# Kernel optimization log

Hardware: AMD Instinct MI355X
Metric: run time of the kernel (lower is better)

## Reference

```python
import jax, jax.numpy as jnp
import numpy as np

B, S, HID, MEM, NW = 32, 256, 1024, 256, 1024
PLAST, IMP = 0.1, 1.0
W_SCALE = 0.02  # sane init for projection weights


def setup_inputs() -> dict:
    key = jax.random.key(0)
    ks = jax.random.split(key, 24)
    n = lambda k, sh, s=1.0: jax.random.normal(k, sh, dtype=jnp.float32) * s
    inp = {
        "q": n(ks[0], (B, S, HID)),
        "data": n(ks[1], (NW, HID)),
        "episodic_k": n(ks[2], (MEM, HID)),
        "episodic_v": n(ks[3], (MEM, HID)),
        "semantic_k": n(ks[4], (MEM, HID)),
        "semantic_v": n(ks[5], (MEM, HID)),
        "working_m": n(ks[6], (1, 10, HID)),
    }
    i = 7
    for name in ("atte", "atts", "attw"):
        inp[name + "_in_w"] = n(ks[i], (3 * HID, HID), W_SCALE); i += 1
        inp[name + "_in_b"] = jnp.zeros((3 * HID,), jnp.float32)
        inp[name + "_out_w"] = n(ks[i], (HID, HID), W_SCALE); i += 1
        inp[name + "_out_b"] = jnp.zeros((HID,), jnp.float32)
    inp["proj_w"] = n(ks[i], (HID, 3 * HID), W_SCALE)
    inp["proj_b"] = jnp.zeros((HID,), jnp.float32)
    return inp


def mha_shared_kv(q, k, v, in_w, in_b, out_w, out_b, n_heads):
    # q: [B,S,H]; k,v: [M,H] (memory bank shared across the batch)
    d = q.shape[-1] // n_heads
    wq, wk, wv = jnp.split(in_w, 3, axis=0)
    bq, bk, bv = jnp.split(in_b, 3)
    Bq, Sq, _ = q.shape
    M = k.shape[0]
    qh = (q @ wq.T + bq).reshape(Bq, Sq, n_heads, d)   # [B,S,h,d]
    kh = (k @ wk.T + bk).reshape(M, n_heads, d)        # [M,h,d]
    vh = (v @ wv.T + bv).reshape(M, n_heads, d)
    scale = 1.0 / jnp.sqrt(jnp.float32(d))
    att = jax.nn.softmax(jnp.einsum('bshd,mhd->bhsm', qh, kh) * scale, axis=-1)
    o = jnp.einsum('bhsm,mhd->bshd', att, vh).reshape(Bq, Sq, -1)
    return o @ out_w.T + out_b


def reference(q, data, episodic_k, episodic_v, semantic_k, semantic_v, working_m,
              atte_in_w, atte_in_b, atte_out_w, atte_out_b,
              atts_in_w, atts_in_b, atts_out_w, atts_out_b,
              attw_in_w, attw_in_b, attw_out_w, attw_out_b,
              proj_w, proj_b):
    # ---- write(data, 'episodic'): softmax-addressed fast-weight update ----
    probs = jax.nn.softmax(data @ episodic_k.T, axis=-1)          # [N,M]
    w = probs * (PLAST * IMP)                                     # [N,M]
    u = w.mean(axis=0)[:, None]                                   # [M,1] mean update strength per slot
    writes = jnp.einsum('nm,nh->mh', w, data) / NW                # mean_n data[n]*w[n,m]
    ek = jax.lax.stop_gradient(episodic_k * (1.0 - u) + writes)   # .data assignment -> no grad
    ev = jax.lax.stop_gradient(episodic_v * (1.0 - u) + writes)
    # ---- read(q): 3 small attentions over memory banks, concat, project ----
    e_r = mha_shared_kv(q, ek, ev, atte_in_w, atte_in_b, atte_out_w, atte_out_b, 16)
    s_r = mha_shared_kv(q, semantic_k, semantic_v, atts_in_w, atts_in_b, atts_out_w, atts_out_b, 16)
    w_r = mha_shared_kv(q, working_m[0], working_m[0], attw_in_w, attw_in_b, attw_out_w, attw_out_b, 8)
    cat = jnp.concatenate((e_r, s_r, w_r), axis=-1)               # [B,S,3H]
    return cat @ proj_w.T + proj_b                                # [B,S,H]
```

## Files before the change

kernel.cpp:

```cpp
#include <hip/hip_runtime.h>
#include <hip/hip_bf16.h>


using bf = __hip_bfloat16;
using short8v = __attribute__((ext_vector_type(8))) short;
using f32x4  = __attribute__((ext_vector_type(4))) float;

#define GLOAD_LDS16(g, l) __builtin_amdgcn_global_load_lds( \
    (const __attribute__((address_space(1))) void*)(g), \
    (__attribute__((address_space(3))) void*)(l), 16, 0, 0)

__device__ inline float bf2f(unsigned short s) {
    union { unsigned u; float f; } c; c.u = ((unsigned)s) << 16; return c.f;
}
__device__ inline unsigned short f2bu(float x) {
    union { float f; unsigned u; } c; c.f = x;
    unsigned r = c.u + 0x7FFF + ((c.u >> 16) & 1);
    return (unsigned short)(r >> 16);
}
__device__ inline void storeC(float* p, float v) { *p = v; }
__device__ inline void storeC(bf* p, float v) { *p = __float2bfloat16(v); }

__global__ __launch_bounds__(256) void gemm_bt(
    const bf* __restrict__ A, int lda,
    const bf* __restrict__ B, int ldb,
    float* __restrict__ part, int M, int N, int K)
{
    __shared__ short As[128 * 64];
    __shared__ short Bs[128 * 64];
    const int nbn = N >> 7;
    const int bm = blockIdx.x / nbn, bn = blockIdx.x % nbn;
    const int t = threadIdx.x;
    const int w = t >> 6, lane = t & 63;
    const int wr = w >> 1, wc = w & 1;
    const int l16 = lane & 15, lhi = lane >> 4;
    const int kc = K / gridDim.y;
    const int kbeg = blockIdx.y * kc, kend = kbeg + kc;

    f32x4 acc[4][4];
    #pragma unroll
    for (int i = 0; i < 4; ++i)
        #pragma unroll
        for (int j = 0; j < 4; ++j) { f32x4 z = {0.f, 0.f, 0.f, 0.f}; acc[i][j] = z; }

    const bf* Arow = A + (size_t)bm * 128 * lda;
    const bf* Brow = B + (size_t)bn * 128 * ldb;

    for (int k0 = kbeg; k0 < kend; k0 += 64) {
        #pragma unroll
        for (int j = 0; j < 4; ++j) {
            int u = (w * 4 + j) * 64 + lane;
            int row = u >> 3, c8 = u & 7;
            int slot = c8 ^ (row & 7);
            GLOAD_LDS16(Brow + (size_t)row * ldb + k0 + slot * 8, &Bs[(w * 4 + j) * 512]);
            GLOAD_LDS16(Arow + (size_t)row * lda + k0 + slot * 8, &As[(w * 4 + j) * 512]);
        }
        __syncthreads();
        #pragma unroll
        for (int kk = 0; kk < 2; ++kk) {
            short8v af[4], bfr[4];
            #pragma unroll
            for (int mt = 0; mt < 4; ++mt) {
                int row = wr * 64 + mt * 16 + l16;
                int slot = (kk * 4 + lhi) ^ (row & 7);
                af[mt] = *(const short8v*)&As[row * 64 + slot * 8];
            }
            #pragma unroll
            for (int nt = 0; nt < 4; ++nt) {
                int row = wc * 64 + nt * 16 + l16;
                int slot = (kk * 4 + lhi) ^ (row & 7);
                bfr[nt] = *(const short8v*)&Bs[row * 64 + slot * 8];
            }
            #pragma unroll
            for (int mt = 0; mt < 4; ++mt)
                #pragma unroll
                for (int nt = 0; nt < 4; ++nt)
                    acc[mt][nt] = __builtin_amdgcn_mfma_f32_16x16x32_bf16(
                        af[mt], bfr[nt], acc[mt][nt], 0, 0, 0);
        }
        __syncthreads();
    }
    #pragma unroll
    for (int mt = 0; mt < 4; ++mt)
        #pragma unroll
        for (int nt = 0; nt < 4; ++nt) {
            int col = bn * 128 + wc * 64 + nt * 16 + l16;
            #pragma unroll
            for (int j = 0; j < 4; ++j) {
                int rowg = bm * 128 + wr * 64 + mt * 16 + lhi * 4 + j;
                part[(size_t)blockIdx.y * M * N + (size_t)rowg * N + col] = acc[mt][nt][j];
            }
        }
}

template <typename CT>
__global__ __launch_bounds__(512) void gemm256(
    const bf* __restrict__ A, int lda,
    const bf* __restrict__ B, int ldb,
    const float* __restrict__ bias,
    CT* __restrict__ C, int ldc,
    int M, int N, int K)
{
    __shared__ short As[256 * 64];
    __shared__ short Bs[128 * 64];
    const int nbn = N >> 7;
    int bid = blockIdx.x;
    bid = (bid & 7) * (gridDim.x >> 3) + (bid >> 3);
    const int bm = bid / nbn, bn = bid % nbn;
    const int t = threadIdx.x;
    const int w = t >> 6, lane = t & 63;
    const int wr = w >> 1, wc = w & 1;
    const int l16 = lane & 15, lhi = lane >> 4;

    f32x4 acc[4][4];
    #pragma unroll
    for (int i = 0; i < 4; ++i)
        #pragma unroll
        for (int j = 0; j < 4; ++j) { f32x4 z = {0.f, 0.f, 0.f, 0.f}; acc[i][j] = z; }

    const bf* Arow = A + (size_t)bm * 256 * lda;
    const bf* Brow = B + (size_t)bn * 128 * ldb;

    for (int k0 = 0; k0 < K; k0 += 64) {
        #pragma unroll
        for (int j = 0; j < 2; ++j) {
            int u = t + (j << 9);
            int row = u >> 3, c8 = u & 7;
            int slot = c8 ^ (row & 7);
            GLOAD_LDS16(Brow + (size_t)row * ldb + k0 + slot * 8, &Bs[(j * 8 + w) * 512]);
        }
        #pragma unroll
        for (int j = 0; j < 4; ++j) {
            int u = t + (j << 9);
            int row = u >> 3, c8 = u & 7;
            int slot = c8 ^ (row & 7);
            GLOAD_LDS16(Arow + (size_t)row * lda + k0 + slot * 8, &As[(j * 8 + w) * 512]);
        }
        __syncthreads();
        #pragma unroll
        for (int kk = 0; kk < 2; ++kk) {
            short8v af[4], bfr[4];
            #pragma unroll
            for (int mt = 0; mt < 4; ++mt) {
                int row = wr * 64 + mt * 16 + l16;
                int slot = (kk * 4 + lhi) ^ (row & 7);
                af[mt] = *(const short8v*)&As[row * 64 + slot * 8];
            }
            #pragma unroll
            for (int nt = 0; nt < 4; ++nt) {
                int row = wc * 64 + nt * 16 + l16;
                int slot = (kk * 4 + lhi) ^ (row & 7);
                bfr[nt] = *(const short8v*)&Bs[row * 64 + slot * 8];
            }
            #pragma unroll
            for (int mt = 0; mt < 4; ++mt)
                #pragma unroll
                for (int nt = 0; nt < 4; ++nt)
                    acc[mt][nt] = __builtin_amdgcn_mfma_f32_16x16x32_bf16(
                        af[mt], bfr[nt], acc[mt][nt], 0, 0, 0);
        }
        __syncthreads();
    }
    #pragma unroll
    for (int mt = 0; mt < 4; ++mt)
        #pragma unroll
        for (int nt = 0; nt < 4; ++nt) {
            int col = bn * 128 + wc * 64 + nt * 16 + l16;
            float bv = bias ? bias[col] : 0.0f;
            #pragma unroll
            for (int j = 0; j < 4; ++j) {
                int rowg = bm * 256 + wr * 64 + mt * 16 + lhi * 4 + j;
                storeC(&C[(size_t)rowg * ldc + col], acc[mt][nt][j] + bv);
            }
        }
}

__global__ __launch_bounds__(512) void gemm256db(
    const bf* __restrict__ A, int lda,
    const bf* __restrict__ B, int ldb,
    const float* __restrict__ bias,
    float* __restrict__ C, int ldc,
    int M, int N, int K)
{
    __shared__ short As0[256 * 64];
    __shared__ short Bs0[128 * 64];
    __shared__ short As1[256 * 64];
    __shared__ short Bs1[128 * 64];
    const int nbn = N >> 7;
    int bid = blockIdx.x;
    bid = (bid & 7) * (gridDim.x >> 3) + (bid >> 3);
    const int bm = bid / nbn, bn = bid % nbn;
    const int t = threadIdx.x;
    const int w = t >> 6, lane = t & 63;
    const int wr = w >> 1, wc = w & 1;
    const int l16 = lane & 15, lhi = lane >> 4;

    f32x4 acc[4][4];
    #pragma unroll
    for (int i = 0; i < 4; ++i)
        #pragma unroll
        for (int j = 0; j < 4; ++j) { f32x4 z = {0.f, 0.f, 0.f, 0.f}; acc[i][j] = z; }

    const bf* Arow = A + (size_t)bm * 256 * lda;
    const bf* Brow = B + (size_t)bn * 128 * ldb;

    auto stage = [&](short* Asd, short* Bsd, int k0) {
        #pragma unroll
        for (int j = 0; j < 2; ++j) {
            int u = t + (j << 9);
            int row = u >> 3, c8 = u & 7;
            int slot = c8 ^ (row & 7);
            GLOAD_LDS16(Brow + (size_t)row * ldb + k0 + slot * 8, &Bsd[(j * 8 + w) * 512]);
        }
        #pragma unroll
        for (int j = 0; j < 4; ++j) {
            int u = t + (j << 9);
            int row = u >> 3, c8 = u & 7;
            int slot = c8 ^ (row & 7);
            GLOAD_LDS16(Arow + (size_t)row * lda + k0 + slot * 8, &Asd[(j * 8 + w) * 512]);
        }
    };
    auto compute = [&](const short* Ass, const short* Bss) {
        #pragma unroll
        for (int kk = 0; kk < 2; ++kk) {
            short8v af[4], bfr[4];
            #pragma unroll
            for (int mt = 0; mt < 4; ++mt) {
                int row = wr * 64 + mt * 16 + l16;
                int slot = (kk * 4 + lhi) ^ (row & 7);
                af[mt] = *(const short8v*)&Ass[row * 64 + slot * 8];
            }
            #pragma unroll
            for (int nt = 0; nt < 4; ++nt) {
                int row = wc * 64 + nt * 16 + l16;
                int slot = (kk * 4 + lhi) ^ (row & 7);
                bfr[nt] = *(const short8v*)&Bss[row * 64 + slot * 8];
            }
            #pragma unroll
            for (int mt = 0; mt < 4; ++mt)
                #pragma unroll
                for (int nt = 0; nt < 4; ++nt)
                    acc[mt][nt] = __builtin_amdgcn_mfma_f32_16x16x32_bf16(
                        af[mt], bfr[nt], acc[mt][nt], 0, 0, 0);
        }
    };

    const int nt_ = K >> 6;
    stage(As0, Bs0, 0);
    stage(As1, Bs1, 64);
    asm volatile("s_waitcnt vmcnt(6)" ::: "memory");
    __builtin_amdgcn_sched_barrier(0);
    __builtin_amdgcn_s_barrier();

    for (int ti = 0; ti < nt_ - 2; ti += 2) {
        compute(As0, Bs0);
        __builtin_amdgcn_s_barrier();
        stage(As0, Bs0, (ti + 2) << 6);
        asm volatile("s_waitcnt vmcnt(6)" ::: "memory");
        __builtin_amdgcn_sched_barrier(0);
        __builtin_amdgcn_s_barrier();
        compute(As1, Bs1);
        __builtin_amdgcn_s_barrier();
        stage(As1, Bs1, (ti + 3) << 6);
        asm volatile("s_waitcnt vmcnt(6)" ::: "memory");
        __builtin_amdgcn_sched_barrier(0);
        __builtin_amdgcn_s_barrier();
    }
    compute(As0, Bs0);
    __builtin_amdgcn_s_barrier();
    asm volatile("s_waitcnt vmcnt(0)" ::: "memory");
    __builtin_amdgcn_sched_barrier(0);
    __builtin_amdgcn_s_barrier();
    compute(As1, Bs1);

    #pragma unroll
    for (int mt = 0; mt < 4; ++mt)
        #pragma unroll
        for (int nt = 0; nt < 4; ++nt) {
            int col = bn * 128 + wc * 64 + nt * 16 + l16;
            float bv = bias ? bias[col] : 0.0f;
            #pragma unroll
            for (int j = 0; j < 4; ++j) {
                int rowg = bm * 256 + wr * 64 + mt * 16 + lhi * 4 + j;
                C[(size_t)rowg * ldc + col] = acc[mt][nt][j] + bv;
            }
        }
}

struct GG { const bf* A; const bf* B; const float* bias; bf* out;
            int lda, ldb, M, N, ldo, xoff; };
struct GG7 { GG g[7]; };

__global__ __launch_bounds__(256) void ggemm(GG7 P)
{
    __shared__ short As[128 * 64];
    __shared__ short Bs[128 * 64];
    const int bid = blockIdx.x;
    int gidx = 0;
    #pragma unroll
    for (int i = 1; i < 7; ++i) if (bid >= P.g[i].xoff) gidx = i;
    const GG d = P.g[gidx];
    const int lb = bid - d.xoff;
    const int nbn = d.N >> 7;
    const int bm = lb / nbn, bn = lb % nbn;
    const int t = threadIdx.x;
    const int w = t >> 6, lane = t & 63;
    const int wr = w >> 1, wc = w & 1;
    const int l16 = lane & 15, lhi = lane >> 4;

    f32x4 acc[4][4];
    #pragma unroll
    for (int i = 0; i < 4; ++i)
        #pragma unroll
        for (int j = 0; j < 4; ++j) { f32x4 z = {0.f, 0.f, 0.f, 0.f}; acc[i][j] = z; }

    const bf* Afrow = d.A + (size_t)bm * 128 * d.lda;
    const bf* Brow  = d.B + (size_t)bn * 128 * d.ldb;

    for (int k0 = 0; k0 < 1024; k0 += 64) {
        #pragma unroll
        for (int j = 0; j < 4; ++j) {
            int u = (w * 4 + j) * 64 + lane;
            int row = u >> 3, c8 = u & 7;
            int slot = c8 ^ (row & 7);
            GLOAD_LDS16(Brow + (size_t)row * d.ldb + k0 + slot * 8, &Bs[(w * 4 + j) * 512]);
            GLOAD_LDS16(Afrow + (size_t)row * d.lda + k0 + slot * 8, &As[(w * 4 + j) * 512]);
        }
        __syncthreads();
        #pragma unroll
        for (int kk = 0; kk < 2; ++kk) {
            short8v af[4], bfr[4];
            #pragma unroll
            for (int mt = 0; mt < 4; ++mt) {
                int row = wr * 64 + mt * 16 + l16;
                int slot = (kk * 4 + lhi) ^ (row & 7);
                af[mt] = *(const short8v*)&As[row * 64 + slot * 8];
            }
            #pragma unroll
            for (int nt = 0; nt < 4; ++nt) {
                int row = wc * 64 + nt * 16 + l16;
                int slot = (kk * 4 + lhi) ^ (row & 7);
                bfr[nt] = *(const short8v*)&Bs[row * 64 + slot * 8];
            }
            #pragma unroll
            for (int mt = 0; mt < 4; ++mt)
                #pragma unroll
                for (int nt = 0; nt < 4; ++nt)
                    acc[mt][nt] = __builtin_amdgcn_mfma_f32_16x16x32_bf16(
                        af[mt], bfr[nt], acc[mt][nt], 0, 0, 0);
        }
        __syncthreads();
    }
    #pragma unroll
    for (int mt = 0; mt < 4; ++mt)
        #pragma unroll
        for (int nt = 0; nt < 4; ++nt) {
            int col = bn * 128 + wc * 64 + nt * 16 + l16;
            float bv = d.bias ? d.bias[col] : 0.0f;
            #pragma unroll
            for (int j = 0; j < 4; ++j) {
                int rowg = bm * 128 + wr * 64 + mt * 16 + lhi * 4 + j;
                d.out[(size_t)rowg * d.ldo + col]
                    = __float2bfloat16(acc[mt][nt][j] + bv);
            }
        }
}

__global__ __launch_bounds__(512) void attn_es(
    bf* Ocat, const bf* __restrict__ khE, const bf* __restrict__ khS,
    const bf* __restrict__ vTE, const bf* __restrict__ vTS)
{
    __shared__ short Ks[256 * 64];
    __shared__ short Vs[64 * 256];
    const int bank = blockIdx.x >> 10;
    const int lbid = blockIdx.x & 1023;
    const bf* kh  = bank ? khS : khE;
    const bf* vhT = bank ? vTS : vTE;
    bf* QO = Ocat + bank * 1024;
    const int qt = lbid >> 4, head = lbid & 15;
    const int t = threadIdx.x, w = t >> 6, lane = t & 63;
    const int l16 = lane & 15, lhi = lane >> 4;
    const float scale = 0.125f;

    #pragma unroll
    for (int j = 0; j < 4; ++j) {
        int ublk = w * 4 + j;
        int u = ublk * 64 + lane;
        { int row = u >> 3, c8 = u & 7;
          int slot = c8 ^ (row & 7);
          GLOAD_LDS16(kh + (size_t)row * 1024 + head * 64 + slot * 8, &Ks[ublk * 512]); }
        { int row = u >> 5, c16 = u & 31;
          int slot = c16 ^ (row & 7);
          GLOAD_LDS16(vhT + (size_t)(head * 64 + row) * 256 + slot * 8, &Vs[ublk * 512]); }
    }
    const int qr = qt * 128 + w * 16 + l16;
    short8v aq0 = *(const short8v*)(QO + (size_t)qr * 3072 + head * 64 + lhi * 8);
    short8v aq1 = *(const short8v*)(QO + (size_t)qr * 3072 + head * 64 + 32 + lhi * 8);
    __syncthreads();

    f32x4 sc[16];
    #pragma unroll
    for (int nt = 0; nt < 16; ++nt) { f32x4 z = {0.f, 0.f, 0.f, 0.f}; sc[nt] = z; }
    #pragma unroll
    for (int nt = 0; nt < 16; ++nt) {
        int row = nt * 16 + l16;
        #pragma unroll
        for (int kk = 0; kk < 2; ++kk) {
            int slot = (kk * 4 + lhi) ^ (row & 7);
            short8v b = *(const short8v*)&Ks[row * 64 + slot * 8];
            sc[nt] = __builtin_amdgcn_mfma_f32_16x16x32_bf16(kk ? aq1 : aq0, b, sc[nt], 0, 0, 0);
        }
    }
    float inv[4];
    #pragma unroll
    for (int j = 0; j < 4; ++j) {
        float m_ = -1e30f;
        #pragma unroll
        for (int nt = 0; nt < 16; ++nt) m_ = fmaxf(m_, sc[nt][j]);
        #pragma unroll
        for (int off = 8; off; off >>= 1) m_ = fmaxf(m_, __shfl_xor(m_, off));
        float s_ = 0.f;
        #pragma unroll
        for (int nt = 0; nt < 16; ++nt) {
            float e = __expf((sc[nt][j] - m_) * scale);
            sc[nt][j] = e; s_ += e;
        }
        #pragma unroll
        for (int off = 8; off; off >>= 1) s_ += __shfl_xor(s_, off);
        inv[j] = 1.0f / s_;
    }
    __syncthreads();

    char* Pw = (char*)Ks + w * 4096;
    f32x4 oa[4];
    #pragma unroll
    for (int nt = 0; nt < 4; ++nt) { f32x4 z = {0.f, 0.f, 0.f, 0.f}; oa[nt] = z; }
    #pragma unroll
    for (int h = 0; h < 2; ++h) {
        #pragma unroll
        for (int nt = 0; nt < 8; ++nt) {
            int colL = nt * 16 + l16;
            #pragma unroll
            for (int j = 0; j < 4; ++j) {
                int row = lhi * 4 + j;
                *(short*)(Pw + row * 256 + ((colL * 2) ^ ((row & 7) << 4)))
                    = (short)f2bu(sc[h * 8 + nt][j] * inv[j]);
            }
        }
        #pragma unroll
        for (int kk = 0; kk < 4; ++kk) {
            short8v a = *(const short8v*)(Pw + l16 * 256 + (((kk * 32 + lhi * 8) * 2) ^ ((l16 & 7) << 4)));
            #pragma unroll
            for (int nt = 0; nt < 4; ++nt) {
                int row = nt * 16 + l16;
                int m = h * 128 + kk * 32 + lhi * 8;
                short8v b = *(const short8v*)((const char*)Vs + row * 512 + ((m * 2) ^ ((row & 7) << 4)));
                oa[nt] = __builtin_amdgcn_mfma_f32_16x16x32_bf16(a, b, oa[nt], 0, 0, 0);
            }
        }
    }
    #pragma unroll
    for (int nt = 0; nt < 4; ++nt)
        #pragma unroll
        for (int j = 0; j < 4; ++j)
            QO[(size_t)(qt * 128 + w * 16 + lhi * 4 + j) * 3072 + head * 64 + nt * 16 + l16]
                = __float2bfloat16(oa[nt][j]);
}

__global__ __launch_bounds__(256) void attn_w(
    bf* QOp, const bf* __restrict__ khw, const bf* __restrict__ vhw)
{
    const int bs = blockIdx.x;
    const int t = threadIdx.x;
    const int head = t >> 5;
    const int dg = head * 128 + (t & 31) * 4;

    ushort4 qv = *(const ushort4*)(QOp + (size_t)bs * 3072 + dg);
    float q0 = bf2f(qv.x), q1 = bf2f(qv.y), q2 = bf2f(qv.z), q3 = bf2f(qv.w);
    float s[10];
    #pragma unroll
    for (int m = 0; m < 10; ++m) {
        ushort4 kv = *(const ushort4*)(khw + (size_t)m * 1024 + dg);
        float pr = q0 * bf2f(kv.x) + q1 * bf2f(kv.y) + q2 * bf2f(kv.z) + q3 * bf2f(kv.w);
        #pragma unroll
        for (int off = 16; off; off >>= 1) pr += __shfl_xor(pr, off);
        s[m] = pr * 0.08838834764831845f;
    }
    float mx = s[0];
    #pragma unroll
    for (int m = 1; m < 10; ++m) mx = fmaxf(mx, s[m]);
    float pp[10], sum = 0.f;
    #pragma unroll
    for (int m = 0; m < 10; ++m) { pp[m] = __expf(s[m] - mx); sum += pp[m]; }
    float inv = 1.0f / sum;
    float o0 = 0, o1 = 0, o2 = 0, o3 = 0;
    #pragma unroll
    for (int m = 0; m < 10; ++m) {
        ushort4 vv = *(const ushort4*)(vhw + (size_t)m * 1024 + dg);
        o0 += pp[m] * bf2f(vv.x); o1 += pp[m] * bf2f(vv.y);
        o2 += pp[m] * bf2f(vv.z); o3 += pp[m] * bf2f(vv.w);
    }
    bf* op = QOp + (size_t)bs * 3072 + dg;
    op[0] = __float2bfloat16(o0 * inv); op[1] = __float2bfloat16(o1 * inv);
    op[2] = __float2bfloat16(o2 * inv); op[3] = __float2bfloat16(o3 * inv);
}

struct CS { const float* src; bf* dst; int voff; };
struct MP {
    CS cs[13];
    const float* tsrc[4]; bf* tdst[4];
    const float* ow[3]; const float* ob[3]; const float* ib[3];
    float* bp;
    const float* inb_e; const float* inb_s; float* bqcat3;
    const float* wm; const float* inw_w; const float* inb_w;
    bf* khw; bf* vhw;
};

__global__ __launch_bounds__(256) void megaprep(MP P)
{
    __shared__ unsigned short tile[64][65];
    const int bid = blockIdx.x;
    const int t = threadIdx.x;
    if (bid < 20224) {
        int gi = bid * 256 + t;
        int gidx = 0;
        #pragma unroll
        for (int i = 1; i < 13; ++i) if (gi >= P.cs[i].voff) gidx = i;
        int i = (gi - P.cs[gidx].voff) * 4;
        float4 v = *(const float4*)(P.cs[gidx].src + i);
        ushort4 o;
        o.x = f2bu(v.x); o.y = f2bu(v.y); o.z = f2bu(v.z); o.w = f2bu(v.w);
        *(ushort4*)((unsigned short*)P.cs[gidx].dst + i) = o;
    } else if (bid < 21248) {
        int lb = bid - 20224;
        int sel = lb >> 8, bb = lb & 255;
        const float* in = P.tsrc[sel];
        bf* outT = P.tdst[sel];
        int bx = bb & 15, by = bb >> 4;
        int r0 = by * 64, c0 = bx * 64;
        int tr = t >> 4, tc4 = (t & 15) * 4;
        #pragma unroll
        for (int i = 0; i < 4; ++i) {
            int r = tr + i * 16;
            float4 v = *(const float4*)(in + (size_t)(r0 + r) * 1024 + c0 + tc4);
            tile[r][tc4 + 0] = f2bu(v.x); tile[r][tc4 + 1] = f2bu(v.y);
            tile[r][tc4 + 2] = f2bu(v.z); tile[r][tc4 + 3] = f2bu(v.w);
        }
        __syncthreads();
        #pragma unroll
        for (int i = 0; i < 4; ++i) {
            int r = tr + i * 16;
            ushort4 v;
            v.x = tile[tc4 + 0][r]; v.y = tile[tc4 + 1][r];
            v.z = tile[tc4 + 2][r]; v.w = tile[tc4 + 3][r];
            *(ushort4*)((unsigned short*)outT + (size_t)(c0 + r) * 1024 + r0 + tc4) = v;
        }
    } else if (bid < 22016) {
        int g = (bid - 21248) * 4 + (t >> 6);
        int lane = t & 63;
        int bank = g >> 10, j = g & 1023;
        const float* ow = P.ow[bank];
        const float* xx = P.ib[bank] + 2048;
        const float* wrow = ow + (size_t)j * 1024;
        float acc = 0.f;
        #pragma unroll
        for (int cc = 0; cc < 4; ++cc) {
            float4 a = *(const float4*)(wrow + lane * 16 + cc * 4);
            float4 x = *(const float4*)(xx + lane * 16 + cc * 4);
            acc += a.x * x.x + a.y * x.y + a.z * x.z + a.w * x.w;
        }
        #pragma unroll
        for (int off = 32; off; off >>= 1) acc += __shfl_xor(acc, off);
        if (lane == 0) P.bp[g] = acc + P.ob[bank][j];
    } else if (bid < 22028) {
        int i = (bid - 22016) * 256 + t;
        if (i < 1024) P.bqcat3[i] = P.inb_e[i];
        else if (i < 2048) P.bqcat3[i] = P.inb_s[i - 1024];
        else P.bqcat3[i] = P.inb_w[i - 2048];
    } else {
        int o = (bid - 22028) * 4 + (t >> 6);
        int lane = t & 63;
        int sel = o >= 10240;
        int o2 = o - sel * 10240;
        int m = o2 >> 10, c = o2 & 1023;
        const float* wrow = P.inw_w + (size_t)(1024 + sel * 1024 + c) * 1024;
        const float* xrow = P.wm + (size_t)m * 1024;
        float acc = 0.f;
        #pragma unroll
        for (int cc = 0; cc < 4; ++cc) {
            float4 a = *(const float4*)(wrow + lane * 16 + cc * 4);
            float4 x = *(const float4*)(xrow + lane * 16 + cc * 4);
            acc += a.x * x.x + a.y * x.y + a.z * x.z + a.w * x.w;
        }
        #pragma unroll
        for (int off = 32; off; off >>= 1) acc += __shfl_xor(acc, off);
        if (lane == 0) {
            float v = acc + (sel ? 0.f : P.inb_w[1024 + c]);
            (sel ? P.vhw : P.khw)[(size_t)m * 1024 + c] = __float2bfloat16(v);
        }
    }
}


__global__ __launch_bounds__(256) void btot_kern(
    const float* __restrict__ bp, const float* __restrict__ pw,
    const float* __restrict__ pb, float* __restrict__ btot)
{
    int j = blockIdx.x * 4 + (threadIdx.x >> 6);
    int lane = threadIdx.x & 63;
    const float* row = pw + (size_t)j * 3072;
    float acc = 0.f;
    #pragma unroll
    for (int it = 0; it < 12; ++it) {
        int c = lane * 4 + it * 256;
        float4 a = *(const float4*)(row + c);
        float4 x = *(const float4*)(bp + c);
        acc += a.x * x.x + a.y * x.y + a.z * x.z + a.w * x.w;
    }
    #pragma unroll
    for (int off = 32; off; off >>= 1) acc += __shfl_xor(acc, off);
    if (lane == 0) btot[j] = acc + pb[j];
}

__global__ __launch_bounds__(256) void write_softmax_p(const float* __restrict__ part,
                                                       bf* __restrict__ wT)
{
    const int n = blockIdx.x, m = threadIdx.x;
    float s = 0.f;
    #pragma unroll
    for (int k = 0; k < 8; ++k) s += part[(size_t)k * 262144 + n * 256 + m];
    float mx = s;
    #pragma unroll
    for (int off = 32; off; off >>= 1) mx = fmaxf(mx, __shfl_xor(mx, off));
    __shared__ float red[4], red2[4];
    int w = threadIdx.x >> 6;
    if ((threadIdx.x & 63) == 0) red[w] = mx;
    __syncthreads();
    mx = fmaxf(fmaxf(red[0], red[1]), fmaxf(red[2], red[3]));
    float e = __expf(s - mx);
    float sm = e;
    #pragma unroll
    for (int off = 32; off; off >>= 1) sm += __shfl_xor(sm, off);
    if ((threadIdx.x & 63) == 0) red2[w] = sm;
    __syncthreads();
    sm = red2[0] + red2[1] + red2[2] + red2[3];
    wT[(size_t)m * 1024 + n] = __float2bfloat16(0.1f * e / sm);
}

__global__ __launch_bounds__(256) void usum_kern(const bf* __restrict__ wT, float* __restrict__ u)
{
    int w = threadIdx.x >> 6, lane = threadIdx.x & 63;
    int m = blockIdx.x * 4 + w;
    const bf* row = wT + (size_t)m * 1024;
    float s = 0.f;
    for (int i = lane; i < 1024; i += 64) s += __bfloat162float(row[i]);
    #pragma unroll
    for (int off = 32; off; off >>= 1) s += __shfl_xor(s, off);
    if (lane == 0) u[m] = s * (1.0f / 1024.0f);
}

__global__ __launch_bounds__(256) void update_fused(
    const float* __restrict__ epk, const float* __restrict__ epv,
    const float* __restrict__ u, const float* __restrict__ part,
    bf* __restrict__ ekb, bf* __restrict__ evb)
{
    int i = blockIdx.x * 256 + threadIdx.x;
    int m = i >> 10;
    float wr = 0.f;
    #pragma unroll
    for (int k = 0; k < 8; ++k) wr += part[(size_t)k * 262144 + i];
    wr *= (1.0f / 1024.0f);
    float f = 1.0f - u[m];
    ekb[i] = __float2bfloat16(epk[i] * f + wr);
    evb[i] = __float2bfloat16(epv[i] * f + wr);
}

extern "C" void kernel_launch(void* const* d_in, const int* in_sizes, int n_in,
                              void* d_out, int out_size, void* d_ws, size_t ws_size,
                              hipStream_t stream)
{
    const float* q     = (const float*)d_in[0];
    const float* data  = (const float*)d_in[1];
    const float* epk   = (const float*)d_in[2];
    const float* epv   = (const float*)d_in[3];
    const float* smk   = (const float*)d_in[4];
    const float* smv   = (const float*)d_in[5];
    const float* wm    = (const float*)d_in[6];
    const float* inw_e = (const float*)d_in[7];  const float* inb_e = (const float*)d_in[8];
    const float* ow_e  = (const float*)d_in[9];  const float* ob_e  = (const float*)d_in[10];
    const float* inw_s = (const float*)d_in[11]; const float* inb_s = (const float*)d_in[12];
    const float* ow_s  = (const float*)d_in[13]; const float* ob_s  = (const float*)d_in[14];
    const float* inw_w = (const float*)d_in[15]; const float* inb_w = (const float*)d_in[16];
    const float* ow_w  = (const float*)d_in[17]; const float* ob_w  = (const float*)d_in[18];
    const float* pw    = (const float*)d_in[19]; const float* pb    = (const float*)d_in[20];
    float* out  = (float*)d_out;
    float* part = (float*)d_out;
    bf* qb  = (bf*)((char*)d_out + 8388608);
    bf* pwb = (bf*)((char*)d_out + 25165824);

    char* p = (char*)d_ws;
    auto alloc = [&](size_t bytes) -> char* {
        char* r = p; p += (bytes + 255) & ~(size_t)255; return r;
    };
    float* u      = (float*)alloc(256 * 4);
    float* bp     = (float*)alloc(3072 * 4);
    float* btot   = (float*)alloc(1024 * 4);
    float* bqcat3 = (float*)alloc(3072 * 4);
    bf* wT     = (bf*)alloc(256 * 1024 * 2);
    bf* dT     = (bf*)alloc((size_t)1024 * 1024 * 2);
    bf* datab  = (bf*)alloc((size_t)1024 * 1024 * 2);
    bf* epkb   = (bf*)alloc(256 * 1024 * 2);
    bf* smkb   = (bf*)alloc(256 * 1024 * 2);
    bf* smvb   = (bf*)alloc(256 * 1024 * 2);
    bf* ekb    = (bf*)alloc(256 * 1024 * 2);
    bf* evb    = (bf*)alloc(256 * 1024 * 2);
    bf* khE    = (bf*)alloc(256 * 1024 * 2);
    bf* khS    = (bf*)alloc(256 * 1024 * 2);
    bf* vTE    = (bf*)alloc((size_t)1024 * 256 * 2);
    bf* vTS    = (bf*)alloc((size_t)1024 * 256 * 2);
    bf* khw    = (bf*)alloc(10 * 1024 * 2);
    bf* vhw    = (bf*)alloc(10 * 1024 * 2);
    bf* Wall   = (bf*)alloc((size_t)3072 * 1024 * 2);
    bf* WkE    = (bf*)alloc((size_t)1024 * 1024 * 2);
    bf* WkS    = (bf*)alloc((size_t)1024 * 1024 * 2);
    bf* WvE    = (bf*)alloc((size_t)1024 * 1024 * 2);
    bf* WvS    = (bf*)alloc((size_t)1024 * 1024 * 2);
    bf* owT0   = (bf*)alloc((size_t)1024 * 1024 * 2);
    bf* owT1   = (bf*)alloc((size_t)1024 * 1024 * 2);
    bf* owT2   = (bf*)alloc((size_t)1024 * 1024 * 2);
    bf* Gcat   = (bf*)alloc((size_t)1024 * 3072 * 2);
    bf* Ocat   = (bf*)alloc((size_t)8192 * 3072 * 2);
    if ((size_t)(p - (char*)d_ws) > ws_size) return;

    {
        MP P;
        CS cs[13] = { {q, qb, 0},
                      {epk,  epkb, 2097152}, {smv, smvb, 2162688},
                      {inw_e, Wall, 2228224},
                      {inw_s, Wall + (size_t)1024 * 1024, 2490368},
                      {inw_w, Wall + (size_t)2048 * 1024, 2752512},
                      {inw_e + (size_t)1024 * 1024, WkE, 3014656},
                      {inw_s + (size_t)1024 * 1024, WkS, 3276800},
                      {data, datab, 3538944},
                      {pw, pwb, 3801088},
                      {smk, smkb, 4587520},
                      {inw_e + (size_t)2048 * 1024, WvE, 4653056},
                      {inw_s + (size_t)2048 * 1024, WvS, 4915200} };
        for (int i = 0; i < 13; ++i) P.cs[i] = cs[i];
        P.tsrc[0] = data; P.tdst[0] = dT;
        P.tsrc[1] = ow_e; P.tdst[1] = owT0;
        P.tsrc[2] = ow_s; P.tdst[2] = owT1;
        P.tsrc[3] = ow_w; P.tdst[3] = owT2;
        P.ow[0] = ow_e; P.ow[1] = ow_s; P.ow[2] = ow_w;
        P.ob[0] = ob_e; P.ob[1] = ob_s; P.ob[2] = ob_w;
        P.ib[0] = inb_e; P.ib[1] = inb_s; P.ib[2] = inb_w;
        P.bp = bp;
        P.inb_e = inb_e; P.inb_s = inb_s; P.bqcat3 = bqcat3;
        P.wm = wm; P.inw_w = inw_w; P.inb_w = inb_w;
        P.khw = khw; P.vhw = vhw;
        megaprep<<<27148, 256, 0, stream>>>(P);
    }
    btot_kern<<<256, 256, 0, stream>>>(bp, pw, pb, btot);

    gemm_bt<<<dim3(16, 8), 256, 0, stream>>>(datab, 1024, epkb, 1024, part, 1024, 256, 1024);
    write_softmax_p<<<1024, 256, 0, stream>>>(part, wT);
    usum_kern<<<64, 256, 0, stream>>>(wT, u);
    gemm_bt<<<dim3(16, 8), 256, 0, stream>>>(wT, 1024, dT, 1024, part, 256, 1024, 1024);
    update_fused<<<1024, 256, 0, stream>>>(epk, epv, u, part, ekb, evb);

    gemm256<bf><<<768, 512, 0, stream>>>(
        qb, 1024, Wall, 1024, bqcat3, Ocat, 3072, 8192, 3072, 1024);

    {
        GG7 G = {{
            { ekb,        WkE,  inb_e + 1024, khE,         1024, 1024,  256, 1024, 1024, 0   },
            { smkb,       WkS,  inb_s + 1024, khS,         1024, 1024,  256, 1024, 1024, 16  },
            { WvE,        evb,  nullptr,      vTE,         1024, 1024, 1024,  256,  256, 32  },
            { WvS,        smvb, nullptr,      vTS,         1024, 1024, 1024,  256,  256, 48  },
            { pwb + 0,    owT0, nullptr,      Gcat + 0,    3072, 1024, 1024, 1024, 3072, 64  },
            { pwb + 1024, owT1, nullptr,      Gcat + 1024, 3072, 1024, 1024, 1024, 3072, 128 },
            { pwb + 2048, owT2, nullptr,      Gcat + 2048, 3072, 1024, 1024, 1024, 3072, 192 },
        }};
        ggemm<<<256, 256, 0, stream>>>(G);
    }

    attn_es<<<2048, 512, 0, stream>>>(Ocat, khE, khS, vTE, vTS);
    attn_w<<<8192, 256, 0, stream>>>(Ocat + 2048, khw, vhw);

    gemm256db<<<256, 512, 0, stream>>>(
        Ocat, 3072, Gcat, 3072, btot, out, 1024, 8192, 1024, 3072);
}
```

Measured before the change: 277.4 us.

## Use double-buffered GEMM for QKV, fuse usum into update, batch attn_w rows

Templates the double-buffered gemm256db kernel on its output type and uses it in place of the single-buffered gemm256 for the large Q projection GEMM, so global loads overlap MFMA work. The separate usum kernel is removed: update_fused now computes each slot's mean weight with a block reduction and applies the update with vectorised loads and stores, one block per memory slot. attn_w processes four rows per block and keeps the key and value registers loaded across them, cutting redundant loads and launching a quarter as many blocks. The cost is higher LDS use in the QKV GEMM, which may lower occupancy.

```diff
diff --git a/kernel.cpp b/kernel.cpp
--- a/kernel.cpp
+++ b/kernel.cpp
@@ -94,92 +94,11 @@
 }
 
 template <typename CT>
-__global__ __launch_bounds__(512) void gemm256(
+__global__ __launch_bounds__(512) void gemm256db(
     const bf* __restrict__ A, int lda,
     const bf* __restrict__ B, int ldb,
     const float* __restrict__ bias,
     CT* __restrict__ C, int ldc,
-    int M, int N, int K)
-{
-    __shared__ short As[256 * 64];
-    __shared__ short Bs[128 * 64];
-    const int nbn = N >> 7;
-    int bid = blockIdx.x;
-    bid = (bid & 7) * (gridDim.x >> 3) + (bid >> 3);
-    const int bm = bid / nbn, bn = bid % nbn;
-    const int t = threadIdx.x;
-    const int w = t >> 6, lane = t & 63;
-    const int wr = w >> 1, wc = w & 1;
-    const int l16 = lane & 15, lhi = lane >> 4;
-
-    f32x4 acc[4][4];
-    #pragma unroll
-    for (int i = 0; i < 4; ++i)
-        #pragma unroll
-        for (int j = 0; j < 4; ++j) { f32x4 z = {0.f, 0.f, 0.f, 0.f}; acc[i][j] = z; }
-
-    const bf* Arow = A + (size_t)bm * 256 * lda;
-    const bf* Brow = B + (size_t)bn * 128 * ldb;
-
-    for (int k0 = 0; k0 < K; k0 += 64) {
-        #pragma unroll
-        for (int j = 0; j < 2; ++j) {
-            int u = t + (j << 9);
-            int row = u >> 3, c8 = u & 7;
-            int slot = c8 ^ (row & 7);
-            GLOAD_LDS16(Brow + (size_t)row * ldb + k0 + slot * 8, &Bs[(j * 8 + w) * 512]);
-        }
-        #pragma unroll
-        for (int j = 0; j < 4; ++j) {
-            int u = t + (j << 9);
-            int row = u >> 3, c8 = u & 7;
-            int slot = c8 ^ (row & 7);
-            GLOAD_LDS16(Arow + (size_t)row * lda + k0 + slot * 8, &As[(j * 8 + w) * 512]);
-        }
-        __syncthreads();
-        #pragma unroll
-        for (int kk = 0; kk < 2; ++kk) {
-            short8v af[4], bfr[4];
-            #pragma unroll
-            for (int mt = 0; mt < 4; ++mt) {
-                int row = wr * 64 + mt * 16 + l16;
-                int slot = (kk * 4 + lhi) ^ (row & 7);
-                af[mt] = *(const short8v*)&As[row * 64 + slot * 8];
-            }
-            #pragma unroll
-            for (int nt = 0; nt < 4; ++nt) {
-                int row = wc * 64 + nt * 16 + l16;
-                int slot = (kk * 4 + lhi) ^ (row & 7);
-                bfr[nt] = *(const short8v*)&Bs[row * 64 + slot * 8];
-            }
-            #pragma unroll
-            for (int mt = 0; mt < 4; ++mt)
-                #pragma unroll
-                for (int nt = 0; nt < 4; ++nt)
-                    acc[mt][nt] = __builtin_amdgcn_mfma_f32_16x16x32_bf16(
-                        af[mt], bfr[nt], acc[mt][nt], 0, 0, 0);
-        }
-        __syncthreads();
-    }
-    #pragma unroll
-    for (int mt = 0; mt < 4; ++mt)
-        #pragma unroll
-        for (int nt = 0; nt < 4; ++nt) {
-            int col = bn * 128 + wc * 64 + nt * 16 + l16;
-            float bv = bias ? bias[col] : 0.0f;
-            #pragma unroll
-            for (int j = 0; j < 4; ++j) {
-                int rowg = bm * 256 + wr * 64 + mt * 16 + lhi * 4 + j;
-                storeC(&C[(size_t)rowg * ldc + col], acc[mt][nt][j] + bv);
-            }
-        }
-}
-
-__global__ __launch_bounds__(512) void gemm256db(
-    const bf* __restrict__ A, int lda,
-    const bf* __restrict__ B, int ldb,
-    const float* __restrict__ bias,
-    float* __restrict__ C, int ldc,
     int M, int N, int K)
 {
     __shared__ short As0[256 * 64];
@@ -282,7 +201,7 @@
             #pragma unroll
             for (int j = 0; j < 4; ++j) {
                 int rowg = bm * 256 + wr * 64 + mt * 16 + lhi * 4 + j;
-                C[(size_t)rowg * ldc + col] = acc[mt][nt][j] + bv;
+                storeC(&C[(size_t)rowg * ldc + col], acc[mt][nt][j] + bv);
             }
         }
 }
@@ -470,39 +389,47 @@
 __global__ __launch_bounds__(256) void attn_w(
     bf* QOp, const bf* __restrict__ khw, const bf* __restrict__ vhw)
 {
-    const int bs = blockIdx.x;
     const int t = threadIdx.x;
     const int head = t >> 5;
     const int dg = head * 128 + (t & 31) * 4;
 
-    ushort4 qv = *(const ushort4*)(QOp + (size_t)bs * 3072 + dg);
-    float q0 = bf2f(qv.x), q1 = bf2f(qv.y), q2 = bf2f(qv.z), q3 = bf2f(qv.w);
-    float s[10];
+    ushort4 kv[10], vv[10];
     #pragma unroll
     for (int m = 0; m < 10; ++m) {
-        ushort4 kv = *(const ushort4*)(khw + (size_t)m * 1024 + dg);
-        float pr = q0 * bf2f(kv.x) + q1 * bf2f(kv.y) + q2 * bf2f(kv.z) + q3 * bf2f(kv.w);
-        #pragma unroll
-        for (int off = 16; off; off >>= 1) pr += __shfl_xor(pr, off);
-        s[m] = pr * 0.08838834764831845f;
-    }
-    float mx = s[0];
-    #pragma unroll
-    for (int m = 1; m < 10; ++m) mx = fmaxf(mx, s[m]);
-    float pp[10], sum = 0.f;
-    #pragma unroll
-    for (int m = 0; m < 10; ++m) { pp[m] = __expf(s[m] - mx); sum += pp[m]; }
-    float inv = 1.0f / sum;
-    float o0 = 0, o1 = 0, o2 = 0, o3 = 0;
-    #pragma unroll
-    for (int m = 0; m < 10; ++m) {
-        ushort4 vv = *(const ushort4*)(vhw + (size_t)m * 1024 + dg);
-        o0 += pp[m] * bf2f(vv.x); o1 += pp[m] * bf2f(vv.y);
-        o2 += pp[m] * bf2f(vv.z); o3 += pp[m] * bf2f(vv.w);
-    }
-    bf* op = QOp + (size_t)bs * 3072 + dg;
-    op[0] = __float2bfloat16(o0 * inv); op[1] = __float2bfloat16(o1 * inv);
-    op[2] = __float2bfloat16(o2 * inv); op[3] = __float2bfloat16(o3 * inv);
+        kv[m] = *(const ushort4*)(khw + (size_t)m * 1024 + dg);
+        vv[m] = *(const ushort4*)(vhw + (size_t)m * 1024 + dg);
+    }
+    #pragma unroll
+    for (int r = 0; r < 4; ++r) {
+        const int bs = blockIdx.x * 4 + r;
+        ushort4 qv = *(const ushort4*)(QOp + (size_t)bs * 3072 + dg);
+        float q0 = bf2f(qv.x), q1 = bf2f(qv.y), q2 = bf2f(qv.z), q3 = bf2f(qv.w);
+        float s[10];
+        #pragma unroll
+        for (int m = 0; m < 10; ++m) {
+            float pr = q0 * bf2f(kv[m].x) + q1 * bf2f(kv[m].y)
+                     + q2 * bf2f(kv[m].z) + q3 * bf2f(kv[m].w);
+            #pragma unroll
+            for (int off = 16; off; off >>= 1) pr += __shfl_xor(pr, off);
+            s[m] = pr * 0.08838834764831845f;
+        }
+        float mx = s[0];
+        #pragma unroll
+        for (int m = 1; m < 10; ++m) mx = fmaxf(mx, s[m]);
+        float pp[10], sum = 0.f;
+        #pragma unroll
+        for (int m = 0; m < 10; ++m) { pp[m] = __expf(s[m] - mx); sum += pp[m]; }
+        float inv = 1.0f / sum;
+        float o0 = 0, o1 = 0, o2 = 0, o3 = 0;
+        #pragma unroll
+        for (int m = 0; m < 10; ++m) {
+            o0 += pp[m] * bf2f(vv[m].x); o1 += pp[m] * bf2f(vv[m].y);
+            o2 += pp[m] * bf2f(vv[m].z); o3 += pp[m] * bf2f(vv[m].w);
+        }
+        bf* op = QOp + (size_t)bs * 3072 + dg;
+        op[0] = __float2bfloat16(o0 * inv); op[1] = __float2bfloat16(o1 * inv);
+        op[2] = __float2bfloat16(o2 * inv); op[3] = __float2bfloat16(o3 * inv);
+    }
 }
 
 struct CS { const float* src; bf* dst; int voff; };
@@ -647,32 +574,37 @@
     wT[(size_t)m * 1024 + n] = __float2bfloat16(0.1f * e / sm);
 }
 
-__global__ __launch_bounds__(256) void usum_kern(const bf* __restrict__ wT, float* __restrict__ u)
-{
-    int w = threadIdx.x >> 6, lane = threadIdx.x & 63;
-    int m = blockIdx.x * 4 + w;
-    const bf* row = wT + (size_t)m * 1024;
-    float s = 0.f;
-    for (int i = lane; i < 1024; i += 64) s += __bfloat162float(row[i]);
-    #pragma unroll
-    for (int off = 32; off; off >>= 1) s += __shfl_xor(s, off);
-    if (lane == 0) u[m] = s * (1.0f / 1024.0f);
-}
-
 __global__ __launch_bounds__(256) void update_fused(
     const float* __restrict__ epk, const float* __restrict__ epv,
-    const float* __restrict__ u, const float* __restrict__ part,
+    const bf* __restrict__ wT, const float* __restrict__ part,
     bf* __restrict__ ekb, bf* __restrict__ evb)
 {
-    int i = blockIdx.x * 256 + threadIdx.x;
-    int m = i >> 10;
-    float wr = 0.f;
-    #pragma unroll
-    for (int k = 0; k < 8; ++k) wr += part[(size_t)k * 262144 + i];
-    wr *= (1.0f / 1024.0f);
-    float f = 1.0f - u[m];
-    ekb[i] = __float2bfloat16(epk[i] * f + wr);
-    evb[i] = __float2bfloat16(epv[i] * f + wr);
+    __shared__ float red[4];
+    const int m = blockIdx.x, t = threadIdx.x;
+    ushort4 wv = *(const ushort4*)((const unsigned short*)wT + (size_t)m * 1024 + t * 4);
+    float s = bf2f(wv.x) + bf2f(wv.y) + bf2f(wv.z) + bf2f(wv.w);
+    #pragma unroll
+    for (int off = 32; off; off >>= 1) s += __shfl_xor(s, off);
+    if ((t & 63) == 0) red[t >> 6] = s;
+    __syncthreads();
+    float f = 1.0f - (red[0] + red[1] + red[2] + red[3]) * (1.0f / 1024.0f);
+    int base = m * 1024 + t * 4;
+    float4 wr = *(const float4*)(part + base);
+    #pragma unroll
+    for (int k = 1; k < 8; ++k) {
+        float4 v = *(const float4*)(part + (size_t)k * 262144 + base);
+        wr.x += v.x; wr.y += v.y; wr.z += v.z; wr.w += v.w;
+    }
+    const float sc = 1.0f / 1024.0f;
+    float4 pk = *(const float4*)(epk + base);
+    float4 pv = *(const float4*)(epv + base);
+    ushort4 ok, ov;
+    ok.x = f2bu(pk.x * f + wr.x * sc); ok.y = f2bu(pk.y * f + wr.y * sc);
+    ok.z = f2bu(pk.z * f + wr.z * sc); ok.w = f2bu(pk.w * f + wr.w * sc);
+    ov.x = f2bu(pv.x * f + wr.x * sc); ov.y = f2bu(pv.y * f + wr.y * sc);
+    ov.z = f2bu(pv.z * f + wr.z * sc); ov.w = f2bu(pv.w * f + wr.w * sc);
+    *(ushort4*)((unsigned short*)ekb + base) = ok;
+    *(ushort4*)((unsigned short*)evb + base) = ov;
 }
 
 extern "C" void kernel_launch(void* const* d_in, const int* in_sizes, int n_in,
@@ -731,6 +663,7 @@
     bf* Gcat   = (bf*)alloc((size_t)1024 * 3072 * 2);
     bf* Ocat   = (bf*)alloc((size_t)8192 * 3072 * 2);
     if ((size_t)(p - (char*)d_ws) > ws_size) return;
+    (void)u;
 
     {
         MP P;
@@ -764,11 +697,10 @@
 
     gemm_bt<<<dim3(16, 8), 256, 0, stream>>>(datab, 1024, epkb, 1024, part, 1024, 256, 1024);
     write_softmax_p<<<1024, 256, 0, stream>>>(part, wT);
-    usum_kern<<<64, 256, 0, stream>>>(wT, u);
     gemm_bt<<<dim3(16, 8), 256, 0, stream>>>(wT, 1024, dT, 1024, part, 256, 1024, 1024);
-    update_fused<<<1024, 256, 0, stream>>>(epk, epv, u, part, ekb, evb);
-
-    gemm256<bf><<<768, 512, 0, stream>>>(
+    update_fused<<<256, 256, 0, stream>>>(epk, epv, wT, part, ekb, evb);
+
+    gemm256db<bf><<<768, 512, 0, stream>>>(
         qb, 1024, Wall, 1024, bqcat3, Ocat, 3072, 8192, 3072, 1024);
 
     {
@@ -785,8 +717,8 @@
     }
 
     attn_es<<<2048, 512, 0, stream>>>(Ocat, khE, khS, vTE, vTS);
-    attn_w<<<8192, 256, 0, stream>>>(Ocat + 2048, khw, vhw);
-
-    gemm256db<<<256, 512, 0, stream>>>(
+    attn_w<<<2048, 256, 0, stream>>>(Ocat + 2048, khw, vhw);
+
+    gemm256db<float><<<256, 512, 0, stream>>>(
         Ocat, 3072, Gcat, 3072, btot, out, 1024, 8192, 1024, 3072);
 }
```

Result: no change. 280.9 us (+1.2%).
